# Kernel optimization log

Hardware: AMD Instinct MI355X
Metric: run time of the kernel (lower is better)

## Reference

```python
import jax, jax.numpy as jnp
import numpy as np

GROUPS = 32
EPS = 1e-5


def setup_inputs() -> dict:
    key = jax.random.key(0)
    ks = jax.random.split(key, 4)
    B, C, H, W = 32, 512, 32, 32
    x = jax.random.normal(ks[0], (B, C, H, W), dtype=jnp.float32)
    gn_gamma = jnp.ones((C,), jnp.float32)
    gn_beta = jnp.zeros((C,), jnp.float32)
    qkv_w = jax.random.normal(ks[1], (3 * C, C), dtype=jnp.float32) * 0.02
    qkv_b = jnp.zeros((3 * C,), jnp.float32)
    proj_w = jax.random.normal(ks[2], (C, C), dtype=jnp.float32) * 0.02
    proj_b = jnp.zeros((C,), jnp.float32)
    return {"x": x, "gn_gamma": gn_gamma, "gn_beta": gn_beta,
            "qkv_w": qkv_w, "qkv_b": qkv_b, "proj_w": proj_w, "proj_b": proj_b}


def group_norm(x, gamma, beta):
    B, C, H, W = x.shape
    xr = x.reshape(B, GROUPS, C // GROUPS, H, W)
    mean = xr.mean(axis=(2, 3, 4), keepdims=True)
    var = xr.var(axis=(2, 3, 4), keepdims=True)
    xn = ((xr - mean) * jax.lax.rsqrt(var + EPS)).reshape(B, C, H, W)
    return xn * gamma[None, :, None, None] + beta[None, :, None, None]


def reference(x, gn_gamma, gn_beta, qkv_w, qkv_b, proj_w, proj_b):
    B, C, H, W = x.shape
    h_in = group_norm(x, gn_gamma, gn_beta)
    # 1x1 conv == per-pixel matmul over channels
    qkv = jnp.einsum('oc,bchw->bohw', qkv_w, h_in) + qkv_b[None, :, None, None]
    q, k, v = jnp.split(qkv, 3, axis=1)
    scale = 1.0 / jnp.sqrt(jnp.sqrt(jnp.float32(C)))  # 1/sqrt(sqrt(C)), applied to q and k
    attn = jnp.einsum('bchw,bcij->bhwij', q * scale, k * scale)  # [B,H,W,H,W]
    attn = jax.nn.softmax(attn, axis=-1)  # faithful: softmax over last axis (j) only
    h = jnp.einsum('bhwij,bcij->bchw', attn, v)
    h = jnp.einsum('oc,bchw->bohw', proj_w, h) + proj_b[None, :, None, None]
    return x + h
```

## Files before the change

### kernel.cpp

```cpp
#include <hip/hip_runtime.h>

typedef __attribute__((ext_vector_type(8))) short short8;
typedef __attribute__((ext_vector_type(4))) float f32x4;

__device__ __forceinline__ float b2f(unsigned short u) {
  union { unsigned u32; float f; } x; x.u32 = ((unsigned)u) << 16; return x.f;
}
__device__ __forceinline__ unsigned short f2bf(float f) {
  union { float f; unsigned u; } x; x.f = f;
  unsigned r = x.u + 0x7fffu + ((x.u >> 16) & 1u);
  return (unsigned short)(r >> 16);
}
__device__ __forceinline__ void async_load16(const void* g, void* l) {
  __builtin_amdgcn_global_load_lds(
      (__attribute__((address_space(1))) void*)(void*)(g),
      (__attribute__((address_space(3))) void*)(l), 16, 0, 0);
}

__global__ __launch_bounds__(256) void cvt_k(const float* __restrict__ in,
                                             unsigned short* __restrict__ out, int n4) {
  int i = blockIdx.x * 256 + threadIdx.x;
  if (i < n4) {
    float4 v = ((const float4*)in)[i];
    unsigned short o[4] __attribute__((aligned(8)));
    o[0] = f2bf(v.x); o[1] = f2bf(v.y); o[2] = f2bf(v.z); o[3] = f2bf(v.w);
    ((int2*)out)[i] = *(int2*)o;
  }
}

__global__ __launch_bounds__(256) void groupnorm_k(
    const float* __restrict__ x, const float* __restrict__ gamma,
    const float* __restrict__ beta, unsigned short* __restrict__ hin) {
  const int b = blockIdx.x >> 5, g = blockIdx.x & 31;
  const float* xb = x + ((unsigned long long)b * 512ull + (unsigned long long)g * 16ull) * 1024ull;
  const int t = threadIdx.x;
  float4 xr[16];
  float s = 0.f, ss = 0.f;
#pragma unroll
  for (int c = 0; c < 16; ++c) {
    xr[c] = *(const float4*)(xb + c * 1024 + t * 4);
    s += xr[c].x + xr[c].y + xr[c].z + xr[c].w;
    ss += xr[c].x * xr[c].x + xr[c].y * xr[c].y + xr[c].z * xr[c].z + xr[c].w * xr[c].w;
  }
#pragma unroll
  for (int o = 32; o; o >>= 1) { s += __shfl_down(s, o); ss += __shfl_down(ss, o); }
  __shared__ float sred[8];
  if ((t & 63) == 0) { sred[t >> 6] = s; sred[4 + (t >> 6)] = ss; }
  __syncthreads();
  s = sred[0] + sred[1] + sred[2] + sred[3];
  ss = sred[4] + sred[5] + sred[6] + sred[7];
  const float mean = s * (1.f / 16384.f);
  const float rstd = rsqrtf(ss * (1.f / 16384.f) - mean * mean + 1e-5f);
  float ga[16], be[16];
#pragma unroll
  for (int c = 0; c < 16; ++c) {
    float gg = gamma[g * 16 + c] * rstd;
    ga[c] = gg;
    be[c] = beta[g * 16 + c] - mean * gg;
  }
#pragma unroll
  for (int p4 = 0; p4 < 4; ++p4) {
    unsigned short ov[16] __attribute__((aligned(16)));
#pragma unroll
    for (int c = 0; c < 16; ++c)
      ov[c] = f2bf(((const float*)&xr[c])[p4] * ga[c] + be[c]);
    unsigned short* dst = hin + ((unsigned long long)b * 1024ull + t * 4 + p4) * 512ull + g * 16;
    *(int4*)dst = *(int4*)ov;
    *(int4*)(dst + 8) = *(int4*)(ov + 8);
  }
}

template <int MODE, int MI>
__global__ __launch_bounds__(256, 2) void gemm_k(
    const unsigned short* __restrict__ A, unsigned long long sA, int lda,
    const unsigned short* __restrict__ B, unsigned long long sB, int ldb,
    const float* __restrict__ bias, const float* __restrict__ xres,
    unsigned short* __restrict__ out0, unsigned short* __restrict__ out1,
    unsigned short* __restrict__ out2, float* __restrict__ fout,
    float scale, int K) {
  constexpr int MBLK = MI * 32;
  constexpr int SMEM_SHORTS = (MODE == 1) ? (128 * 136) : (MBLK * 32 + 4096);
  __shared__ unsigned short smem[SMEM_SHORTS];
  unsigned short* As = smem;
  unsigned short* Bs = smem + MBLK * 32;
  const int tid = threadIdx.x;
  const int wave = tid >> 6, lane = tid & 63;

  int n_t, m_t, b;
  if (MODE == 0) {
    const int L = blockIdx.x + gridDim.x * (blockIdx.y + gridDim.y * blockIdx.z);
    const int r8 = L & 7, q = L >> 3;
    n_t = q % 12;
    const int mb = (q / 12) * 8 + r8;
    m_t = mb & 3;
    b = mb >> 2;
  } else if (MODE == 1) {
    const int L = blockIdx.x + gridDim.x * (blockIdx.y + gridDim.y * blockIdx.z);
    const int slice = L & 7, t = L >> 3;
    b = slice * 4 + (t >> 6);
    const int rem = t & 63;
    m_t = rem >> 3;
    n_t = rem & 7;
  } else if (MODE == 2) {
    const int L = blockIdx.x + gridDim.x * (blockIdx.y + gridDim.y * blockIdx.z);
    const int slice = L & 7, t = L >> 3;
    b = slice * 4 + (t >> 4);
    const int rem = t & 15;
    m_t = rem >> 2;
    n_t = rem & 3;
  } else {
    n_t = blockIdx.x; m_t = blockIdx.y; b = blockIdx.z;
  }
  const int m0 = m_t * MBLK, n0 = n_t * 128;
  const int wm = (wave & 1) * (MI * 16), wn = (wave >> 1) * 64;
  const unsigned short* Ab = A + (unsigned long long)b * sA + (unsigned long long)m0 * lda;
  const unsigned short* Bb = B + (unsigned long long)b * sB + (unsigned long long)n0 * ldb;

  f32x4 acc[MI][4];
#pragma unroll
  for (int i = 0; i < MI; ++i)
#pragma unroll
    for (int j = 0; j < 4; ++j)
#pragma unroll
      for (int r = 0; r < 4; ++r) acc[i][j][r] = 0.f;

  const int lrow = lane & 15;
  const int lk = lane >> 4;
  const int srow = lane >> 2;
  const int scol = (((lane & 3) ^ ((lane >> 3) & 3)) << 3);
  const int swz = (lrow >> 1) & 3;

  for (int kt = 0; kt < K; kt += 32) {
    {
      const unsigned short* ga = Ab + kt + (unsigned long long)(wave * 16 + srow) * lda + scol;
#pragma unroll
      for (int c = 0; c < MI / 2; ++c)
        async_load16(ga + (unsigned long long)(c * 64) * lda, (void*)(As + (wave + 4 * c) * 512));
      const unsigned short* gb = Bb + kt + (unsigned long long)(wave * 16 + srow) * ldb + scol;
      async_load16(gb, (void*)(Bs + wave * 512));
      async_load16(gb + 64ull * (unsigned long long)ldb, (void*)(Bs + (wave + 4) * 512));
    }
    __syncthreads();
    short8 af[MI], bfr[4];
#pragma unroll
    for (int i = 0; i < MI; ++i)
      af[i] = *(const short8*)(As + (wm + i * 16 + lrow) * 32 + ((lk ^ swz) << 3));
#pragma unroll
    for (int i = 0; i < 4; ++i)
      bfr[i] = *(const short8*)(Bs + (wn + i * 16 + lrow) * 32 + ((lk ^ swz) << 3));
#pragma unroll
    for (int mi = 0; mi < MI; ++mi)
#pragma unroll
      for (int ni = 0; ni < 4; ++ni)
        acc[mi][ni] = __builtin_amdgcn_mfma_f32_16x16x32_bf16(af[mi], bfr[ni], acc[mi][ni], 0, 0, 0);
    __syncthreads();
  }

  const int r0 = lk * 4;
  const int cn = lrow;

  if (MODE == 0) {
    const int which = n0 >> 9;
#pragma unroll
    for (int ni = 0; ni < 4; ++ni) {
      const int o = n0 + wn + ni * 16 + cn;
      const float bi = bias[o];
      const int oin = o & 511;
      if (which < 2) {
        unsigned short* dst = (which == 0 ? out0 : out1) + (unsigned long long)b * 524288ull;
#pragma unroll
        for (int mi = 0; mi < MI; ++mi) {
          const int pbase = m0 + wm + mi * 16 + r0;
#pragma unroll
          for (int r = 0; r < 4; ++r)
            dst[(unsigned long long)(pbase + r) * 512ull + oin] = f2bf((acc[mi][ni][r] + bi) * scale);
        }
      } else {
        unsigned short* dst = out2 + (unsigned long long)b * 524288ull + (unsigned long long)oin * 1024ull;
#pragma unroll
        for (int mi = 0; mi < MI; ++mi) {
          const int pbase = m0 + wm + mi * 16 + r0;
          unsigned short h4[4] __attribute__((aligned(8)));
#pragma unroll
          for (int r = 0; r < 4; ++r) h4[r] = f2bf(acc[mi][ni][r] + bi);
          *(int2*)(dst + pbase) = *(int2*)h4;
        }
      }
    }
  } else if (MODE == 1) {
#pragma unroll
    for (int mi = 0; mi < MI; ++mi)
#pragma unroll
      for (int ni = 0; ni < 4; ++ni)
#pragma unroll
        for (int r = 0; r < 4; ++r) acc[mi][ni][r] = __expf(acc[mi][ni][r]);
    float inv[4][MI / 2];
#pragma unroll
    for (int ni = 0; ni < 4; ++ni)
#pragma unroll
      for (int cp = 0; cp < MI / 2; ++cp) {
        float s8 = 0.f;
#pragma unroll
        for (int mm = 0; mm < 2; ++mm)
#pragma unroll
          for (int r = 0; r < 4; ++r) s8 += acc[cp * 2 + mm][ni][r];
        s8 += __shfl_xor(s8, 16);
        s8 += __shfl_xor(s8, 32);
        inv[ni][cp] = 1.f / s8;
      }
    unsigned short* Pt = smem;
#pragma unroll
    for (int mi = 0; mi < MI; ++mi)
#pragma unroll
      for (int ni = 0; ni < 4; ++ni) {
        unsigned short p4[4] __attribute__((aligned(8)));
#pragma unroll
        for (int r = 0; r < 4; ++r) p4[r] = f2bf(acc[mi][ni][r] * inv[ni][mi >> 1]);
        const int li = wn + ni * 16 + cn;
        const int lj = wm + mi * 16 + r0;
        *(int2*)(Pt + li * 136 + lj) = *(int2*)p4;
      }
    __syncthreads();
    unsigned short* dst = out0 + (unsigned long long)b * 1048576ull;
#pragma unroll
    for (int pass = 0; pass < 8; ++pass) {
      const int row = pass * 16 + (tid >> 4);
      const int col = (tid & 15) * 8;
      int4 v = *(const int4*)(Pt + row * 136 + col);
      *(int4*)(dst + (unsigned long long)(n0 + row) * 1024ull + m0 + col) = v;
    }
  } else if (MODE == 2) {
    unsigned short* dst = out0 + (unsigned long long)b * 524288ull;
#pragma unroll
    for (int mi = 0; mi < MI; ++mi) {
      const int ib = m0 + wm + mi * 16 + r0;
#pragma unroll
      for (int ni = 0; ni < 4; ++ni) {
        const int c = n0 + wn + ni * 16 + cn;
#pragma unroll
        for (int r = 0; r < 4; ++r)
          dst[(unsigned long long)(ib + r) * 512ull + c] = f2bf(acc[mi][ni][r]);
      }
    }
  } else {
    float* dst = fout + (unsigned long long)b * 524288ull;
    const float* xr = xres + (unsigned long long)b * 524288ull;
#pragma unroll
    for (int mi = 0; mi < MI; ++mi) {
      const int ob = m0 + wm + mi * 16 + r0;
#pragma unroll
      for (int r = 0; r < 4; ++r) {
        const int o = ob + r;
        const float bi = bias[o];
#pragma unroll
        for (int ni = 0; ni < 4; ++ni) {
          const int p = n0 + wn + ni * 16 + cn;
          const unsigned long long idx = (unsigned long long)o * 1024ull + p;
          dst[idx] = acc[mi][ni][r] + bi + xr[idx];
        }
      }
    }
  }
}

extern "C" void kernel_launch(void* const* d_in, const int* in_sizes, int n_in,
                              void* d_out, int out_size, void* d_ws, size_t ws_size,
                              hipStream_t stream) {
  const float* x     = (const float*)d_in[0];
  const float* gamma = (const float*)d_in[1];
  const float* beta  = (const float*)d_in[2];
  const float* qkvw  = (const float*)d_in[3];
  const float* qkvb  = (const float*)d_in[4];
  const float* projw = (const float*)d_in[5];
  const float* projb = (const float*)d_in[6];
  float* out = (float*)d_out;
  char* ws = (char*)d_ws;

  unsigned short* Hin = (unsigned short*)(ws);
  unsigned short* Q   = (unsigned short*)(ws + 1ull * 33554432ull);
  unsigned short* Kb  = (unsigned short*)(ws + 2ull * 33554432ull);
  unsigned short* V   = (unsigned short*)(ws + 3ull * 33554432ull);
  unsigned short* S   = (unsigned short*)(ws + 4ull * 33554432ull);
  unsigned short* Wq  = (unsigned short*)(ws + 6ull * 33554432ull);
  unsigned short* Wp  = (unsigned short*)(ws + 6ull * 33554432ull + 2ull * 1048576ull);
  unsigned short* H   = Hin;

  const float SCALE = 0.21022410381342864f;
  dim3 blk(256);
  const float* nzf = nullptr;
  unsigned short* nzo = nullptr;
  float* nzfo = nullptr;

  hipLaunchKernelGGL(cvt_k, dim3(768), blk, 0, stream, qkvw, Wq, 196608);
  hipLaunchKernelGGL(cvt_k, dim3(256), blk, 0, stream, projw, Wp, 65536);
  hipLaunchKernelGGL(groupnorm_k, dim3(1024), blk, 0, stream, x, gamma, beta, Hin);
  hipLaunchKernelGGL((gemm_k<0, 8>), dim3(12, 4, 32), blk, 0, stream,
                     Hin, 524288ull, 512, Wq, 0ull, 512, qkvb, nzf, Q, Kb, V, nzfo, SCALE, 512);
  hipLaunchKernelGGL((gemm_k<1, 4>), dim3(8, 8, 32), blk, 0, stream,
                     Kb, 524288ull, 512, Q, 524288ull, 512, nzf, nzf, S, nzo, nzo, nzfo, 0.f, 512);
  hipLaunchKernelGGL((gemm_k<2, 8>), dim3(4, 4, 32), blk, 0, stream,
                     S, 1048576ull, 1024, V, 524288ull, 1024, nzf, nzf, H, nzo, nzo, nzfo, 0.f, 1024);
  hipLaunchKernelGGL((gemm_k<3, 8>), dim3(8, 2, 32), blk, 0, stream,
                     Wp, 0ull, 512, H, 524288ull, 512, projb, x, nzo, nzo, nzo, out, 0.f, 512);
}
```

Baseline: 350.2 us.

## Double GEMM K-tile to 64 with XOR-swizzled LDS layout and merge weight casts

Each GEMM mainloop iteration now stages a 64-wide K slice instead of 32. It uses an 8-way XOR swizzle on the LDS rows and runs two MFMA sub-steps per load. This halves the number of barrier pairs and loop iterations, giving each sync more compute to cover its latency, at the cost of doubling the LDS footprint per block, which may cut occupancy. The two fp32-to-bf16 weight conversion kernels are also merged into one launch to save a kernel launch.

```diff
diff --git a/kernel.cpp b/kernel.cpp
--- a/kernel.cpp
+++ b/kernel.cpp
@@ -17,15 +17,18 @@
       (__attribute__((address_space(3))) void*)(l), 16, 0, 0);
 }
 
-__global__ __launch_bounds__(256) void cvt_k(const float* __restrict__ in,
-                                             unsigned short* __restrict__ out, int n4) {
+__global__ __launch_bounds__(256) void cvt2_k(
+    const float* __restrict__ a, unsigned short* __restrict__ oa, int n4a,
+    const float* __restrict__ bsrc, unsigned short* __restrict__ ob, int n4b) {
   int i = blockIdx.x * 256 + threadIdx.x;
-  if (i < n4) {
-    float4 v = ((const float4*)in)[i];
-    unsigned short o[4] __attribute__((aligned(8)));
-    o[0] = f2bf(v.x); o[1] = f2bf(v.y); o[2] = f2bf(v.z); o[3] = f2bf(v.w);
-    ((int2*)out)[i] = *(int2*)o;
-  }
+  const float* src; unsigned short* dst; int idx;
+  if (i < n4a) { src = a; dst = oa; idx = i; }
+  else if (i < n4a + n4b) { src = bsrc; dst = ob; idx = i - n4a; }
+  else return;
+  float4 v = ((const float4*)src)[idx];
+  unsigned short o[4] __attribute__((aligned(8)));
+  o[0] = f2bf(v.x); o[1] = f2bf(v.y); o[2] = f2bf(v.z); o[3] = f2bf(v.w);
+  ((int2*)dst)[idx] = *(int2*)o;
 }
 
 __global__ __launch_bounds__(256) void groupnorm_k(
@@ -79,10 +82,13 @@
     unsigned short* __restrict__ out2, float* __restrict__ fout,
     float scale, int K) {
   constexpr int MBLK = MI * 32;
-  constexpr int SMEM_SHORTS = (MODE == 1) ? (128 * 136) : (MBLK * 32 + 4096);
+  constexpr int STAGE_SHORTS = MBLK * 64 + 128 * 64;
+  constexpr int SMEM_SHORTS = (MODE == 1)
+      ? ((STAGE_SHORTS > 128 * 136) ? STAGE_SHORTS : 128 * 136)
+      : STAGE_SHORTS;
   __shared__ unsigned short smem[SMEM_SHORTS];
   unsigned short* As = smem;
-  unsigned short* Bs = smem + MBLK * 32;
+  unsigned short* Bs = smem + MBLK * 64;
   const int tid = threadIdx.x;
   const int wave = tid >> 6, lane = tid & 63;
 
@@ -126,33 +132,42 @@
 
   const int lrow = lane & 15;
   const int lk = lane >> 4;
-  const int srow = lane >> 2;
-  const int scol = (((lane & 3) ^ ((lane >> 3) & 3)) << 3);
-  const int swz = (lrow >> 1) & 3;
-
-  for (int kt = 0; kt < K; kt += 32) {
+  const int sr = lane >> 3;
+  const int pc = (((lane & 7) ^ sr) << 3);
+  const int r7 = lrow & 7;
+
+  for (int kt = 0; kt < K; kt += 64) {
     {
-      const unsigned short* ga = Ab + kt + (unsigned long long)(wave * 16 + srow) * lda + scol;
-#pragma unroll
-      for (int c = 0; c < MI / 2; ++c)
-        async_load16(ga + (unsigned long long)(c * 64) * lda, (void*)(As + (wave + 4 * c) * 512));
-      const unsigned short* gb = Bb + kt + (unsigned long long)(wave * 16 + srow) * ldb + scol;
-      async_load16(gb, (void*)(Bs + wave * 512));
-      async_load16(gb + 64ull * (unsigned long long)ldb, (void*)(Bs + (wave + 4) * 512));
+#pragma unroll
+      for (int c = 0; c < MBLK / 32; ++c) {
+        const int row = wave * (MBLK / 4) + c * 8;
+        async_load16(Ab + kt + (unsigned long long)(row + sr) * lda + pc,
+                     (void*)(As + row * 64));
+      }
+#pragma unroll
+      for (int c = 0; c < 4; ++c) {
+        const int row = wave * 32 + c * 8;
+        async_load16(Bb + kt + (unsigned long long)(row + sr) * ldb + pc,
+                     (void*)(Bs + row * 64));
+      }
     }
     __syncthreads();
-    short8 af[MI], bfr[4];
-#pragma unroll
-    for (int i = 0; i < MI; ++i)
-      af[i] = *(const short8*)(As + (wm + i * 16 + lrow) * 32 + ((lk ^ swz) << 3));
-#pragma unroll
-    for (int i = 0; i < 4; ++i)
-      bfr[i] = *(const short8*)(Bs + (wn + i * 16 + lrow) * 32 + ((lk ^ swz) << 3));
-#pragma unroll
-    for (int mi = 0; mi < MI; ++mi)
-#pragma unroll
-      for (int ni = 0; ni < 4; ++ni)
-        acc[mi][ni] = __builtin_amdgcn_mfma_f32_16x16x32_bf16(af[mi], bfr[ni], acc[mi][ni], 0, 0, 0);
+#pragma unroll
+    for (int ks = 0; ks < 2; ++ks) {
+      const int ko = (((ks << 2) + lk) ^ r7) << 3;
+      short8 af[MI], bfr[4];
+#pragma unroll
+      for (int i = 0; i < MI; ++i)
+        af[i] = *(const short8*)(As + (wm + i * 16 + lrow) * 64 + ko);
+#pragma unroll
+      for (int i = 0; i < 4; ++i)
+        bfr[i] = *(const short8*)(Bs + (wn + i * 16 + lrow) * 64 + ko);
+#pragma unroll
+      for (int mi = 0; mi < MI; ++mi)
+#pragma unroll
+        for (int ni = 0; ni < 4; ++ni)
+          acc[mi][ni] = __builtin_amdgcn_mfma_f32_16x16x32_bf16(af[mi], bfr[ni], acc[mi][ni], 0, 0, 0);
+    }
     __syncthreads();
   }
 
@@ -291,8 +306,7 @@
   unsigned short* nzo = nullptr;
   float* nzfo = nullptr;
 
-  hipLaunchKernelGGL(cvt_k, dim3(768), blk, 0, stream, qkvw, Wq, 196608);
-  hipLaunchKernelGGL(cvt_k, dim3(256), blk, 0, stream, projw, Wp, 65536);
+  hipLaunchKernelGGL(cvt2_k, dim3(1024), blk, 0, stream, qkvw, Wq, 196608, projw, Wp, 65536);
   hipLaunchKernelGGL(groupnorm_k, dim3(1024), blk, 0, stream, x, gamma, beta, Hin);
   hipLaunchKernelGGL((gemm_k<0, 8>), dim3(12, 4, 32), blk, 0, stream,
                      Hin, 524288ull, 512, Wq, 0ull, 512, qkvb, nzf, Q, Kb, V, nzfo, SCALE, 512);
```

Result: faster. 321.0 us (-8.3%).
